# Kernel tuning notes

Measured on AMD Instinct MI355X. Metric: run time of the kernel, lower is better.

Reference implementation:

```python
import jax, jax.numpy as jnp
import numpy as np


def euler2mat(omega):
    # omega: [3] Euler angles (x, y, z); R = Rz @ Ry @ Rx
    sx, sy, sz = jnp.sin(omega[0]), jnp.sin(omega[1]), jnp.sin(omega[2])
    cx, cy, cz = jnp.cos(omega[0]), jnp.cos(omega[1]), jnp.cos(omega[2])
    Rx = jnp.array([[1.0, 0.0, 0.0], [0.0, cx, -sx], [0.0, sx, cx]], dtype=omega.dtype)
    Ry = jnp.array([[cy, 0.0, sy], [0.0, 1.0, 0.0], [-sy, 0.0, cy]], dtype=omega.dtype)
    Rz = jnp.array([[cz, -sz, 0.0], [sz, cz, 0.0], [0.0, 0.0, 1.0]], dtype=omega.dtype)
    return Rz @ Ry @ Rx


def cd_loss(pred, gt):
    # pred: [N,3], gt: [K,3] -> mean over N of min_k ||pred_n - gt_k||^2
    a = jnp.sum(pred * pred, axis=1)[:, None]          # [N,1]
    b = jnp.sum(gt * gt, axis=1)[None, :]              # [1,K]
    c = jnp.einsum('ik,jk->ij', pred, gt)              # [N,K]
    dist = a + b - 2.0 * c                             # [N,K]
    return jnp.mean(jnp.min(dist, axis=1))


def setup_inputs() -> dict:
    key = jax.random.key(0)
    k1, k2, k3, k4 = jax.random.split(key, 4)
    return {
        "visual_points": jax.random.normal(k1, (16384, 3), dtype=jnp.float32),
        "tactile_points": jax.random.normal(k2, (2048, 3), dtype=jnp.float32),
        "model_points": jax.random.normal(k3, (8192, 3), dtype=jnp.float32),
        "scale": jnp.ones((), dtype=jnp.float32),
        "state": jax.random.normal(k4, (6,), dtype=jnp.float32),
    }


def reference(visual_points, tactile_points, model_points, scale, state):
    t = state[0:3]                 # translation [3]
    r = euler2mat(state[3:6])      # rotation [3,3]
    vc = ((visual_points - t[None, :]) @ r) / scale
    tc = ((tactile_points - t[None, :]) @ r) / scale
    E = 1.0 * cd_loss(vc, model_points) + 0.1 * cd_loss(tc, model_points)
    return E
```

## Files before the change

kernel.cpp:

```cpp
#include <hip/hip_runtime.h>
#include <hip/hip_bf16.h>

#define NVIS   16384
#define NTAC   2048
#define NPRED  (NVIS + NTAC)
#define NMODEL 8192

#define BLK    256
#define PPT    3
#define TILE   (BLK * PPT)
#define NTILE  (NPRED / TILE)
#define CHUNK  256
#define NCHUNK (NMODEL / CHUNK)

#define BIGF     3.4e38f
#define INF_BITS 0x7F800000u



__global__ __launch_bounds__(BLK) void cd_setup_kernel(
    const float* __restrict__ model,
    const float* __restrict__ scale,
    const float* __restrict__ state,
    float4* __restrict__ model4,
    unsigned* __restrict__ pmin)
{
    const int tid = threadIdx.x;
    const int bid = blockIdx.x;

    if (bid < NMODEL / BLK) {
        const float ax = state[3], ay = state[4], az = state[5];
        const float sx = sinf(ax), cx = cosf(ax);
        const float sy = sinf(ay), cy = cosf(ay);
        const float sz = sinf(az), cz = cosf(az);
        const float R00 = cz * cy;
        const float R01 = cz * sy * sx - sz * cx;
        const float R02 = cz * sy * cx + sz * sx;
        const float R10 = sz * cy;
        const float R11 = sz * sy * sx + cz * cx;
        const float R12 = sz * sy * cx - cz * sx;
        const float R20 = -sy;
        const float R21 = cy * sx;
        const float R22 = cy * cx;
        const float t0 = state[0], t1 = state[1], t2 = state[2];
        const float s  = scale[0];

        const int mid = bid * BLK + tid;
        const float* mp = model + 3 * mid;
        const float mx = mp[0], my = mp[1], mz = mp[2];
        const float wx = fmaf(s, mx * R00 + my * R01 + mz * R02, t0);
        const float wy = fmaf(s, mx * R10 + my * R11 + mz * R12, t1);
        const float wz = fmaf(s, mx * R20 + my * R21 + mz * R22, t2);
        model4[mid] = make_float4(wx, wy, wz, 0.5f * (wx * wx + wy * wy + wz * wz));
    } else {
        const int pid = (bid - NMODEL / BLK) * BLK + tid;
        pmin[pid] = INF_BITS;
    }
}

__global__ __launch_bounds__(BLK) void cd_partial_kernel(
    const float* __restrict__ vis,
    const float* __restrict__ tac,
    const float4* __restrict__ model4,
    unsigned* __restrict__ pmin)
{
    const int tid   = threadIdx.x;
    const int tile  = blockIdx.x;
    const int chunk = blockIdx.y;

    float nx[PPT], ny[PPT], nz[PPT], pa[PPT];
    #pragma unroll
    for (int k = 0; k < PPT; ++k) {
        const int pid = tile * TILE + k * BLK + tid;
        const float* pp = (pid < NVIS) ? (vis + 3 * pid) : (tac + 3 * (pid - NVIS));
        const float p0 = pp[0], p1 = pp[1], p2 = pp[2];
        pa[k] = p0 * p0 + p1 * p1 + p2 * p2;
        nx[k] = -p0; ny[k] = -p1; nz[k] = -p2;
    }

    const float4* __restrict__ mrow = model4 + chunk * CHUNK;

    float b0 = BIGF, b1 = BIGF, b2 = BIGF;
    #pragma unroll 8
    for (int j = 0; j < CHUNK; ++j) {
        const float4 m = mrow[j];
        b0 = fminf(b0, fmaf(nx[0], m.x, fmaf(ny[0], m.y, fmaf(nz[0], m.z, m.w))));
        b1 = fminf(b1, fmaf(nx[1], m.x, fmaf(ny[1], m.y, fmaf(nz[1], m.z, m.w))));
        b2 = fminf(b2, fmaf(nx[2], m.x, fmaf(ny[2], m.y, fmaf(nz[2], m.z, m.w))));
    }

    const int pbase = tile * TILE + tid;
    atomicMin(&pmin[pbase + 0 * BLK], __float_as_uint(fmaf(2.0f, b0, pa[0])));
    atomicMin(&pmin[pbase + 1 * BLK], __float_as_uint(fmaf(2.0f, b1, pa[1])));
    atomicMin(&pmin[pbase + 2 * BLK], __float_as_uint(fmaf(2.0f, b2, pa[2])));
}

__global__ __launch_bounds__(BLK) void cd_reduce_kernel(
    const unsigned* __restrict__ pmin,
    const float* __restrict__ scale,
    float* __restrict__ out)
{
    const int tid = threadIdx.x;
    const int pid = blockIdx.x * BLK + tid;

    float v = __uint_as_float(pmin[pid]);
    #pragma unroll
    for (int off = 32; off > 0; off >>= 1)
        v += __shfl_down(v, off, 64);

    __shared__ float sh[BLK / 64];
    if ((tid & 63) == 0) sh[tid >> 6] = v;
    __syncthreads();

    if (tid == 0) {
        const float s = scale[0];
        const float inv2 = 1.0f / (s * s);
        const float t = sh[0] + sh[1] + sh[2] + sh[3];
        const float scaled = (blockIdx.x < NVIS / BLK) ? t * inv2 * (1.0f / (float)NVIS)
                                                       : t * inv2 * (0.1f / (float)NTAC);
        atomicAdd(out, scaled);
    }
}

extern "C" void kernel_launch(void* const* d_in, const int* in_sizes, int n_in,
                              void* d_out, int out_size, void* d_ws, size_t ws_size,
                              hipStream_t stream) {
    const float* vis   = (const float*)d_in[0];
    const float* tac   = (const float*)d_in[1];
    const float* model = (const float*)d_in[2];
    const float* scale = (const float*)d_in[3];
    const float* state = (const float*)d_in[4];
    float* out = (float*)d_out;

    float4*   model4 = (float4*)d_ws;
    unsigned* pmin   = (unsigned*)(model4 + NMODEL);

    hipMemsetAsync(out, 0, sizeof(float), stream);

    cd_setup_kernel<<<NMODEL / BLK + NPRED / BLK, BLK, 0, stream>>>(
        model, scale, state, model4, pmin);

    dim3 grid(NTILE, NCHUNK);
    cd_partial_kernel<<<grid, BLK, 0, stream>>>(vis, tac, model4, pmin);

    cd_reduce_kernel<<<NPRED / BLK, BLK, 0, stream>>>(pmin, scale, out);
}
```

Baseline: 87.10 us.

## Fuse model transform into partial kernel via LDS and single-block final reduce

Removes the separate setup kernel. Each partial block now transforms its own 256-point model chunk into shared memory and reads it from LDS in the inner loop, instead of reading a precomputed float4 buffer from global memory. The pmin buffer is initialized with a memset to all ones, and the final reduce runs as one 1024-thread block that writes the output directly, with no atomicAdd and no output memset. This cuts the launch count and global traffic, at the cost of redundant sin/cos and transform work in every block plus a barrier per block.

```diff
diff --git a/kernel.cpp b/kernel.cpp
--- a/kernel.cpp
+++ b/kernel.cpp
@@ -13,22 +13,24 @@
 #define CHUNK  256
 #define NCHUNK (NMODEL / CHUNK)
 
-#define BIGF     3.4e38f
-#define INF_BITS 0x7F800000u
+#define BIGF   3.4e38f
 
 
-
-__global__ __launch_bounds__(BLK) void cd_setup_kernel(
+__global__ __launch_bounds__(BLK) void cd_partial_kernel(
+    const float* __restrict__ vis,
+    const float* __restrict__ tac,
     const float* __restrict__ model,
     const float* __restrict__ scale,
     const float* __restrict__ state,
-    float4* __restrict__ model4,
     unsigned* __restrict__ pmin)
 {
-    const int tid = threadIdx.x;
-    const int bid = blockIdx.x;
+    __shared__ float4 sm[CHUNK];
 
-    if (bid < NMODEL / BLK) {
+    const int tid   = threadIdx.x;
+    const int tile  = blockIdx.x;
+    const int chunk = blockIdx.y;
+
+    {
         const float ax = state[3], ay = state[4], az = state[5];
         const float sx = sinf(ax), cx = cosf(ax);
         const float sy = sinf(ay), cy = cosf(ay);
@@ -45,28 +47,13 @@
         const float t0 = state[0], t1 = state[1], t2 = state[2];
         const float s  = scale[0];
 
-        const int mid = bid * BLK + tid;
-        const float* mp = model + 3 * mid;
+        const float* mp = model + 3 * (chunk * CHUNK + tid);
         const float mx = mp[0], my = mp[1], mz = mp[2];
         const float wx = fmaf(s, mx * R00 + my * R01 + mz * R02, t0);
         const float wy = fmaf(s, mx * R10 + my * R11 + mz * R12, t1);
         const float wz = fmaf(s, mx * R20 + my * R21 + mz * R22, t2);
-        model4[mid] = make_float4(wx, wy, wz, 0.5f * (wx * wx + wy * wy + wz * wz));
-    } else {
-        const int pid = (bid - NMODEL / BLK) * BLK + tid;
-        pmin[pid] = INF_BITS;
+        sm[tid] = make_float4(wx, wy, wz, 0.5f * (wx * wx + wy * wy + wz * wz));
     }
-}
-
-__global__ __launch_bounds__(BLK) void cd_partial_kernel(
-    const float* __restrict__ vis,
-    const float* __restrict__ tac,
-    const float4* __restrict__ model4,
-    unsigned* __restrict__ pmin)
-{
-    const int tid   = threadIdx.x;
-    const int tile  = blockIdx.x;
-    const int chunk = blockIdx.y;
 
     float nx[PPT], ny[PPT], nz[PPT], pa[PPT];
     #pragma unroll
@@ -78,12 +65,12 @@
         nx[k] = -p0; ny[k] = -p1; nz[k] = -p2;
     }
 
-    const float4* __restrict__ mrow = model4 + chunk * CHUNK;
+    __syncthreads();
 
     float b0 = BIGF, b1 = BIGF, b2 = BIGF;
     #pragma unroll 8
     for (int j = 0; j < CHUNK; ++j) {
-        const float4 m = mrow[j];
+        const float4 m = sm[j];
         b0 = fminf(b0, fmaf(nx[0], m.x, fmaf(ny[0], m.y, fmaf(nz[0], m.z, m.w))));
         b1 = fminf(b1, fmaf(nx[1], m.x, fmaf(ny[1], m.y, fmaf(nz[1], m.z, m.w))));
         b2 = fminf(b2, fmaf(nx[2], m.x, fmaf(ny[2], m.y, fmaf(nz[2], m.z, m.w))));
@@ -95,30 +82,38 @@
     atomicMin(&pmin[pbase + 2 * BLK], __float_as_uint(fmaf(2.0f, b2, pa[2])));
 }
 
-__global__ __launch_bounds__(BLK) void cd_reduce_kernel(
+__global__ __launch_bounds__(1024) void cd_reduce_kernel(
     const unsigned* __restrict__ pmin,
     const float* __restrict__ scale,
     float* __restrict__ out)
 {
     const int tid = threadIdx.x;
-    const int pid = blockIdx.x * BLK + tid;
 
-    float v = __uint_as_float(pmin[pid]);
+    float vs = 0.0f, ts = 0.0f;
     #pragma unroll
-    for (int off = 32; off > 0; off >>= 1)
-        v += __shfl_down(v, off, 64);
+    for (int it = 0; it < NPRED / 1024; ++it) {
+        const int pid = it * 1024 + tid;
+        const float v = __uint_as_float(pmin[pid]);
+        if (pid < NVIS) vs += v; else ts += v;
+    }
 
-    __shared__ float sh[BLK / 64];
-    if ((tid & 63) == 0) sh[tid >> 6] = v;
+    #pragma unroll
+    for (int off = 32; off > 0; off >>= 1) {
+        vs += __shfl_down(vs, off, 64);
+        ts += __shfl_down(ts, off, 64);
+    }
+
+    __shared__ float svis[16], stac[16];
+    if ((tid & 63) == 0) { svis[tid >> 6] = vs; stac[tid >> 6] = ts; }
     __syncthreads();
 
     if (tid == 0) {
+        float v = 0.0f, t = 0.0f;
+        #pragma unroll
+        for (int w = 0; w < 16; ++w) { v += svis[w]; t += stac[w]; }
         const float s = scale[0];
         const float inv2 = 1.0f / (s * s);
-        const float t = sh[0] + sh[1] + sh[2] + sh[3];
-        const float scaled = (blockIdx.x < NVIS / BLK) ? t * inv2 * (1.0f / (float)NVIS)
-                                                       : t * inv2 * (0.1f / (float)NTAC);
-        atomicAdd(out, scaled);
+        out[0] = inv2 * (v * (1.0f / (float)NVIS) + t * (0.1f / (float)NTAC));
     }
 }
 
@@ -132,16 +127,12 @@
     const float* state = (const float*)d_in[4];
     float* out = (float*)d_out;
 
-    float4*   model4 = (float4*)d_ws;
-    unsigned* pmin   = (unsigned*)(model4 + NMODEL);
+    unsigned* pmin = (unsigned*)d_ws;
 
-    hipMemsetAsync(out, 0, sizeof(float), stream);
-
-    cd_setup_kernel<<<NMODEL / BLK + NPRED / BLK, BLK, 0, stream>>>(
-        model, scale, state, model4, pmin);
+    hipMemsetAsync(pmin, 0xFF, NPRED * sizeof(unsigned), stream);
 
     dim3 grid(NTILE, NCHUNK);
-    cd_partial_kernel<<<grid, BLK, 0, stream>>>(vis, tac, model4, pmin);
+    cd_partial_kernel<<<grid, BLK, 0, stream>>>(vis, tac, model, scale, state, pmin);
 
-    cd_reduce_kernel<<<NPRED / BLK, BLK, 0, stream>>>(pmin, scale, out);
+    cd_reduce_kernel<<<1, 1024, 0, stream>>>(pmin, scale, out);
 }
```

Result: faster. 78.47 us (-9.9%).
